# Optimization experiments

Measured on AMD Instinct MI355X. Metric: run time of the kernel, lower is better.

The kernel has to match this reference:

```python
import jax, jax.numpy as jnp
import numpy as np

NEG_SLOPE = 0.2  # PyG GATv2Conv default negative_slope


def gatv2_conv(x, src, dst, Wl, bl, Wr, br, att, bias, concat=True):
    # x: [N, Fin]; src/dst: [E] (message flows src -> dst, softmax over dst)
    N = x.shape[0]
    H, C = att.shape
    xl = (x @ Wl + bl).reshape(N, H, C)  # source-side transform (lin_l)
    xr = (x @ Wr + br).reshape(N, H, C)  # target-side transform (lin_r)
    e = xl[src] + xr[dst]                              # [E, H, C]
    score = jnp.sum(jax.nn.leaky_relu(e, NEG_SLOPE) * att, axis=-1)  # [E, H]
    # segment softmax over incoming edges of each target node
    m = jax.ops.segment_max(score, dst, num_segments=N)               # [N, H]
    a = jnp.exp(score - m[dst])
    denom = jax.ops.segment_sum(a, dst, num_segments=N)               # [N, H]
    alpha = a / denom[dst]                                            # [E, H]
    out = jax.ops.segment_sum(xl[src] * alpha[..., None], dst, num_segments=N)  # [N, H, C]
    if concat:
        out = out.reshape(N, H * C)
    else:
        out = out.mean(axis=1)
    return out + bias


def setup_inputs() -> dict:
    key = jax.random.key(0)
    ks = jax.random.split(key, 12)
    N, E, Fin = 100000, 1600000, 128
    H1, C1 = 8, 16
    C2 = 64
    def glorot(k, shape):
        fan_in, fan_out = shape[0], shape[-1]
        lim = (6.0 / (fan_in + fan_out)) ** 0.5
        return jax.random.uniform(k, shape, jnp.float32, -lim, lim)
    x = jax.random.normal(ks[0], (N, Fin), jnp.float32)
    edge_index = jax.random.randint(ks[1], (2, E), 0, N, dtype=jnp.int64)
    return {
        "x": x,
        "edge_index": edge_index,
        "Wl1": glorot(ks[2], (Fin, H1 * C1)),
        "bl1": jnp.zeros((H1 * C1,), jnp.float32),
        "Wr1": glorot(ks[3], (Fin, H1 * C1)),
        "br1": jnp.zeros((H1 * C1,), jnp.float32),
        "att1": glorot(ks[4], (H1, C1)),
        "bias1": jnp.zeros((H1 * C1,), jnp.float32),
        "Wl2": glorot(ks[5], (H1 * C1, C2)),
        "bl2": jnp.zeros((C2,), jnp.float32),
        "Wr2": glorot(ks[6], (H1 * C1, C2)),
        "br2": jnp.zeros((C2,), jnp.float32),
        "att2": glorot(ks[7], (1, C2)),
        "bias2": jnp.zeros((C2,), jnp.float32),
    }


def reference(x, edge_index, Wl1, bl1, Wr1, br1, att1, bias1,
              Wl2, bl2, Wr2, br2, att2, bias2):
    N = x.shape[0]
    loops = jnp.arange(N, dtype=edge_index.dtype)
    src = jnp.concatenate([edge_index[0], loops])  # PyG adds self loops by default
    dst = jnp.concatenate([edge_index[1], loops])
    # eval mode: F.dropout(training=False) is identity
    h = gatv2_conv(x, src, dst, Wl1, bl1, Wr1, br1, att1, bias1, concat=True)
    h = jax.nn.elu(h)
    out = gatv2_conv(h, src, dst, Wl2, bl2, Wr2, br2, att2, bias2, concat=True)
    return out
```

## Files before the change

kernel.cpp:

```cpp
#include <hip/hip_runtime.h>
#include <math.h>

#define FIN 128
#define F1  128
#define C2  64
#define NEG 0.2f

#define BKT_SHIFT 8
#define BKT_SIZE  256
#define SCAT_CHUNK 8192
#define IMGCAP 8192

typedef _Float16 half4 __attribute__((ext_vector_type(4)));
typedef _Float16 f16x8 __attribute__((ext_vector_type(8)));
typedef _Float16 h2    __attribute__((ext_vector_type(2)));
typedef float    f32x4 __attribute__((ext_vector_type(4)));

union H8u { f16x8 v; h2 p[4]; };

__device__ __forceinline__ float lrelu(float z) { return fmaxf(z, NEG * z); }

__global__ __launch_bounds__(256) void bucket_hist_kernel(
    const int* __restrict__ ei, int* __restrict__ bcnt, int E, int ET, int NBKT) {
  __shared__ int sh[512];
  const int t = threadIdx.x;
  for (int b = t; b < NBKT; b += 256) sh[b] = 0;
  __syncthreads();
  const int g0 = blockIdx.x * SCAT_CHUNK + t;
#pragma unroll
  for (int i = 0; i < 32; ++i) {
    const int g = g0 + i * 256;
    if (g < ET) {
      const int dst = (g < E) ? ei[E + g] : (g - E);
      atomicAdd(&sh[dst >> BKT_SHIFT], 1);
    }
  }
  __syncthreads();
  for (int b = t; b < NBKT; b += 256)
    if (sh[b]) atomicAdd(&bcnt[b], sh[b]);
}

__global__ __launch_bounds__(512) void bucket_scan_kernel(
    const int* __restrict__ bcnt, int* __restrict__ bbase, int* __restrict__ bcur,
    int* __restrict__ indptr, int NBKT, int N, int ET) {
  __shared__ int sh[512];
  const int t = threadIdx.x;
  const int v = (t < NBKT) ? bcnt[t] : 0;
  sh[t] = v;
  __syncthreads();
  for (int off = 1; off < 512; off <<= 1) {
    int val = (t >= off) ? sh[t - off] : 0;
    __syncthreads();
    sh[t] += val;
    __syncthreads();
  }
  const int excl = sh[t] - v;
  if (t < NBKT) { bbase[t] = excl; bcur[t] = excl; }
  if (t == NBKT - 1) bbase[NBKT] = excl + v;
  if (t == 0) indptr[N] = ET;
}

__global__ __launch_bounds__(256) void bucket_scatter_kernel(
    const int* __restrict__ ei, int* __restrict__ bcur, int* __restrict__ tmp,
    int E, int ET, int NBKT) {
  __shared__ int sh_hist[512];
  __shared__ int sh_base[512];
  const int t = threadIdx.x;
  for (int b = t; b < NBKT; b += 256) sh_hist[b] = 0;
  __syncthreads();
  const int g0 = blockIdx.x * SCAT_CHUNK + t;
  int bk[32], pk[32];
#pragma unroll
  for (int i = 0; i < 32; ++i) {
    const int g = g0 + i * 256;
    int b = -1, p = 0;
    if (g < ET) {
      const int src = (g < E) ? ei[g] : (g - E);
      const int dst = (g < E) ? ei[E + g] : (g - E);
      b = dst >> BKT_SHIFT;
      p = (src << BKT_SHIFT) | (dst & (BKT_SIZE - 1));
      atomicAdd(&sh_hist[b], 1);
    }
    bk[i] = b; pk[i] = p;
  }
  __syncthreads();
  for (int b = t; b < NBKT; b += 256) {
    const int c = sh_hist[b];
    sh_base[b] = c ? atomicAdd(&bcur[b], c) : 0;
    sh_hist[b] = 0;
  }
  __syncthreads();
#pragma unroll
  for (int i = 0; i < 32; ++i) {
    if (bk[i] >= 0) {
      const int off = atomicAdd(&sh_hist[bk[i]], 1);
      tmp[sh_base[bk[i]] + off] = pk[i];
    }
  }
}

__global__ __launch_bounds__(256) void build_csr_kernel(
    const int* __restrict__ tmp, const int* __restrict__ bbase,
    int* __restrict__ indptr, int* __restrict__ csr, int N) {
  __shared__ int cnt[256];
  __shared__ int cur[256];
  __shared__ int img[IMGCAP];
  const int b = blockIdx.x;
  const int t = threadIdx.x;
  const int base = bbase[b];
  const int cntb = bbase[b + 1] - base;
  cnt[t] = 0;
  __syncthreads();
  for (int i = t; i < cntb; i += 256)
    atomicAdd(&cnt[tmp[base + i] & (BKT_SIZE - 1)], 1);
  __syncthreads();
  const int v = cnt[t];
  cur[t] = v;
  __syncthreads();
  for (int off = 1; off < 256; off <<= 1) {
    int val = (t >= off) ? cur[t - off] : 0;
    __syncthreads();
    cur[t] += val;
    __syncthreads();
  }
  const int excl = cur[t] - v;
  const int node = (b << BKT_SHIFT) + t;
  if (node < N) indptr[node] = base + excl;
  __syncthreads();
  cur[t] = excl;
  __syncthreads();
  if (cntb <= IMGCAP) {
    for (int i = t; i < cntb; i += 256) {
      const int p = tmp[base + i];
      const int pos = atomicAdd(&cur[p & (BKT_SIZE - 1)], 1);
      img[pos] = p >> BKT_SHIFT;
    }
    __syncthreads();
    for (int i = t; i < cntb; i += 256) csr[base + i] = img[i];
  } else {
    for (int i = t; i < cntb; i += 256) {
      const int p = tmp[base + i];
      const int pos = atomicAdd(&cur[p & (BKT_SIZE - 1)], 1);
      csr[base + pos] = p >> BKT_SHIFT;
    }
  }
}

__global__ __launch_bounds__(256) void conv_fp16_kernel(
    const float* __restrict__ src, _Float16* __restrict__ dst, int n4) {
  const int i = blockIdx.x * 256 + threadIdx.x;
  if (i < n4) {
    const float4 v = ((const float4*)src)[i];
    half4 h;
    h.x = (_Float16)v.x; h.y = (_Float16)v.y;
    h.z = (_Float16)v.z; h.w = (_Float16)v.w;
    ((half4*)dst)[i] = h;
  }
}

__global__ __launch_bounds__(256) void wtrans_kernel(
    const float* __restrict__ W0, const float* __restrict__ W1,
    const float* __restrict__ W2, const float* __restrict__ W3,
    _Float16* __restrict__ T0, _Float16* __restrict__ T1,
    _Float16* __restrict__ T2, _Float16* __restrict__ T3) {
  const int m = blockIdx.y;
  const float* W = (m == 0) ? W0 : (m == 1) ? W1 : (m == 2) ? W2 : W3;
  _Float16* T = (m == 0) ? T0 : (m == 1) ? T1 : (m == 2) ? T2 : T3;
  const int ncols = (m < 2) ? 128 : 64;
  const int idx = blockIdx.x * 256 + threadIdx.x;
  if (idx < ncols * 128) {
    const int n = idx >> 7;
    const int k = idx & 127;
    T[idx] = (_Float16)W[k * ncols + n];
  }
}

template<int NCOLS, int CPW>
__global__ __launch_bounds__(256) void gemm_mfma_kernel(
    const _Float16* __restrict__ A,
    const _Float16* __restrict__ Wt0, const float* __restrict__ b0, _Float16* __restrict__ O0,
    const _Float16* __restrict__ Wt1, const float* __restrict__ b1, _Float16* __restrict__ O1,
    int M) {
  const int zsel = blockIdx.z;
  const _Float16* Wt = zsel ? Wt1 : Wt0;
  const float* bias  = zsel ? b1 : b0;
  _Float16* O        = zsel ? O1 : O0;
  const int wave = threadIdx.x >> 6;
  const int lane = threadIdx.x & 63;
  const int row16 = lane & 15;
  const int quad  = lane >> 4;
  const int kb = quad * 8;
  f16x8 bfrag[CPW][4];
  float bv[CPW];
#pragma unroll
  for (int c = 0; c < CPW; ++c) {
    const int n0 = (wave * CPW + c) * 16;
    bv[c] = bias[n0 + row16];
#pragma unroll
    for (int kt = 0; kt < 4; ++kt)
      bfrag[c][kt] = *(const f16x8*)(Wt + (n0 + row16) * 128 + kt * 32 + kb);
  }
  const int rowTiles = (M + 15) >> 4;
  for (int rt = blockIdx.x; rt < rowTiles; rt += gridDim.x) {
    const int r0 = rt << 4;
    const int arow = min(r0 + row16, M - 1);
    f16x8 afrag[4];
#pragma unroll
    for (int kt = 0; kt < 4; ++kt)
      afrag[kt] = *(const f16x8*)(A + (size_t)arow * 128 + kt * 32 + kb);
    f32x4 acc[CPW];
#pragma unroll
    for (int c = 0; c < CPW; ++c) acc[c] = (f32x4){0.f, 0.f, 0.f, 0.f};
#pragma unroll
    for (int kt = 0; kt < 4; ++kt)
#pragma unroll
      for (int c = 0; c < CPW; ++c)
        acc[c] = __builtin_amdgcn_mfma_f32_16x16x32_f16(afrag[kt], bfrag[c][kt], acc[c], 0, 0, 0);
#pragma unroll
    for (int c = 0; c < CPW; ++c) {
      const int col = (wave * CPW + c) * 16 + row16;
#pragma unroll
      for (int r = 0; r < 4; ++r) {
        const int row = r0 + quad * 4 + r;
        if (row < M)
          O[(size_t)row * NCOLS + col] = (_Float16)(acc[c][r] + bv[c]);
      }
    }
  }
}

__global__ __launch_bounds__(256) void attn1_kernel(
    const _Float16* __restrict__ xl, const _Float16* __restrict__ xr,
    const float* __restrict__ att, const float* __restrict__ bias,
    const int* __restrict__ indptr, const int* __restrict__ csr,
    _Float16* __restrict__ hout, int N) {
  const int lane = threadIdx.x & 15;
  const int v = blockIdx.x * 16 + (threadIdx.x >> 4);
  if (v >= N) return;
  const int c8 = lane << 3;
  const _Float16* xlp = xl + c8;
  H8u xru; xru.v = *(const f16x8*)(xr + (v << 7) + c8);
  H8u atu;
  {
    const float4 a0 = *(const float4*)(att + c8);
    const float4 a1 = *(const float4*)(att + c8 + 4);
    f16x8 a;
    a[0] = (_Float16)a0.x; a[1] = (_Float16)a0.y; a[2] = (_Float16)a0.z; a[3] = (_Float16)a0.w;
    a[4] = (_Float16)a1.x; a[5] = (_Float16)a1.y; a[6] = (_Float16)a1.z; a[7] = (_Float16)a1.w;
    atu.v = a;
  }
  const h2 neg2 = {(_Float16)NEG, (_Float16)NEG};
  const h2 zero2 = {(_Float16)0.f, (_Float16)0.f};
  const int beg = indptr[v];
  const int end = indptr[v + 1];
  float l = 0.f;
  float acc[8] = {0.f, 0.f, 0.f, 0.f, 0.f, 0.f, 0.f, 0.f};
  int e = beg;
  for (; e + 4 <= end; e += 4) {
    const int s0 = csr[e + 0];
    const int s1 = csr[e + 1];
    const int s2 = csr[e + 2];
    const int s3 = csr[e + 3];
    H8u x0, x1, x2, x3;
    x0.v = *(const f16x8*)(xlp + (s0 << 7));
    x1.v = *(const f16x8*)(xlp + (s1 << 7));
    x2.v = *(const f16x8*)(xlp + (s2 << 7));
    x3.v = *(const f16x8*)(xlp + (s3 << 7));
    h2 sa0 = zero2, sa1 = zero2, sa2 = zero2, sa3 = zero2;
#pragma unroll
    for (int j = 0; j < 4; ++j) {
      h2 e0 = x0.p[j] + xru.p[j];
      h2 e1 = x1.p[j] + xru.p[j];
      h2 e2 = x2.p[j] + xru.p[j];
      h2 e3 = x3.p[j] + xru.p[j];
      e0 = __builtin_elementwise_max(e0, e0 * neg2);
      e1 = __builtin_elementwise_max(e1, e1 * neg2);
      e2 = __builtin_elementwise_max(e2, e2 * neg2);
      e3 = __builtin_elementwise_max(e3, e3 * neg2);
      sa0 = e0 * atu.p[j] + sa0;
      sa1 = e1 * atu.p[j] + sa1;
      sa2 = e2 * atu.p[j] + sa2;
      sa3 = e3 * atu.p[j] + sa3;
    }
    float t0 = (float)sa0[0] + (float)sa0[1];
    float t1 = (float)sa1[0] + (float)sa1[1];
    float t2 = (float)sa2[0] + (float)sa2[1];
    float t3 = (float)sa3[0] + (float)sa3[1];
    t0 += __shfl_xor(t0, 1);  t1 += __shfl_xor(t1, 1);
    t2 += __shfl_xor(t2, 1);  t3 += __shfl_xor(t3, 1);
    const float p0 = __expf(t0);
    const float p1 = __expf(t1);
    const float p2 = __expf(t2);
    const float p3 = __expf(t3);
    l += (p0 + p1) + (p2 + p3);
#pragma unroll
    for (int j = 0; j < 4; ++j) {
      acc[2*j]   = fmaf(p0, (float)x0.p[j][0], acc[2*j]);
      acc[2*j+1] = fmaf(p0, (float)x0.p[j][1], acc[2*j+1]);
      acc[2*j]   = fmaf(p1, (float)x1.p[j][0], acc[2*j]);
      acc[2*j+1] = fmaf(p1, (float)x1.p[j][1], acc[2*j+1]);
      acc[2*j]   = fmaf(p2, (float)x2.p[j][0], acc[2*j]);
      acc[2*j+1] = fmaf(p2, (float)x2.p[j][1], acc[2*j+1]);
      acc[2*j]   = fmaf(p3, (float)x3.p[j][0], acc[2*j]);
      acc[2*j+1] = fmaf(p3, (float)x3.p[j][1], acc[2*j+1]);
    }
  }
  for (; e < end; ++e) {
    const int s = csr[e];
    H8u xv; xv.v = *(const f16x8*)(xlp + (s << 7));
    h2 sa = zero2;
#pragma unroll
    for (int j = 0; j < 4; ++j) {
      h2 ev = xv.p[j] + xru.p[j];
      ev = __builtin_elementwise_max(ev, ev * neg2);
      sa = ev * atu.p[j] + sa;
    }
    float tt = (float)sa[0] + (float)sa[1];
    tt += __shfl_xor(tt, 1);
    const float p = __expf(tt);
    l += p;
#pragma unroll
    for (int j = 0; j < 4; ++j) {
      acc[2*j]   = fmaf(p, (float)xv.p[j][0], acc[2*j]);
      acc[2*j+1] = fmaf(p, (float)xv.p[j][1], acc[2*j+1]);
    }
  }
  const float rl = 1.f / l;
  const float4 b0 = *(const float4*)(bias + c8);
  const float4 b1 = *(const float4*)(bias + c8 + 4);
  float r[8];
  r[0] = fmaf(acc[0], rl, b0.x); r[1] = fmaf(acc[1], rl, b0.y);
  r[2] = fmaf(acc[2], rl, b0.z); r[3] = fmaf(acc[3], rl, b0.w);
  r[4] = fmaf(acc[4], rl, b1.x); r[5] = fmaf(acc[5], rl, b1.y);
  r[6] = fmaf(acc[6], rl, b1.z); r[7] = fmaf(acc[7], rl, b1.w);
  f16x8 hres;
#pragma unroll
  for (int i = 0; i < 8; ++i) {
    const float z = r[i] > 0.f ? r[i] : expm1f(r[i]);
    hres[i] = (_Float16)z;
  }
  *(f16x8*)(hout + (v << 7) + c8) = hres;
}

__global__ __launch_bounds__(256) void attn2_kernel(
    const _Float16* __restrict__ xl, const _Float16* __restrict__ xr,
    const float* __restrict__ att, const float* __restrict__ bias,
    const int* __restrict__ indptr, const int* __restrict__ csr,
    float* __restrict__ out, int N) {
  const int lane = threadIdx.x & 7;
  const int v = blockIdx.x * 32 + (threadIdx.x >> 3);
  if (v >= N) return;
  const int c8 = lane << 3;
  const _Float16* xlp = xl + c8;
  H8u xru; xru.v = *(const f16x8*)(xr + (v << 6) + c8);
  H8u atu;
  {
    const float4 a0 = *(const float4*)(att + c8);
    const float4 a1 = *(const float4*)(att + c8 + 4);
    f16x8 a;
    a[0] = (_Float16)a0.x; a[1] = (_Float16)a0.y; a[2] = (_Float16)a0.z; a[3] = (_Float16)a0.w;
    a[4] = (_Float16)a1.x; a[5] = (_Float16)a1.y; a[6] = (_Float16)a1.z; a[7] = (_Float16)a1.w;
    atu.v = a;
  }
  const h2 neg2 = {(_Float16)NEG, (_Float16)NEG};
  const h2 zero2 = {(_Float16)0.f, (_Float16)0.f};
  const int beg = indptr[v];
  const int end = indptr[v + 1];
  float l = 0.f;
  float acc[8] = {0.f, 0.f, 0.f, 0.f, 0.f, 0.f, 0.f, 0.f};
  int e = beg;
  for (; e + 4 <= end; e += 4) {
    const int s0 = csr[e + 0];
    const int s1 = csr[e + 1];
    const int s2 = csr[e + 2];
    const int s3 = csr[e + 3];
    H8u x0, x1, x2, x3;
    x0.v = *(const f16x8*)(xlp + (s0 << 6));
    x1.v = *(const f16x8*)(xlp + (s1 << 6));
    x2.v = *(const f16x8*)(xlp + (s2 << 6));
    x3.v = *(const f16x8*)(xlp + (s3 << 6));
    h2 sa0 = zero2, sa1 = zero2, sa2 = zero2, sa3 = zero2;
#pragma unroll
    for (int j = 0; j < 4; ++j) {
      h2 e0 = x0.p[j] + xru.p[j];
      h2 e1 = x1.p[j] + xru.p[j];
      h2 e2 = x2.p[j] + xru.p[j];
      h2 e3 = x3.p[j] + xru.p[j];
      e0 = __builtin_elementwise_max(e0, e0 * neg2);
      e1 = __builtin_elementwise_max(e1, e1 * neg2);
      e2 = __builtin_elementwise_max(e2, e2 * neg2);
      e3 = __builtin_elementwise_max(e3, e3 * neg2);
      sa0 = e0 * atu.p[j] + sa0;
      sa1 = e1 * atu.p[j] + sa1;
      sa2 = e2 * atu.p[j] + sa2;
      sa3 = e3 * atu.p[j] + sa3;
    }
    float t0 = (float)sa0[0] + (float)sa0[1];
    float t1 = (float)sa1[0] + (float)sa1[1];
    float t2 = (float)sa2[0] + (float)sa2[1];
    float t3 = (float)sa3[0] + (float)sa3[1];
    t0 += __shfl_xor(t0, 1);  t1 += __shfl_xor(t1, 1);
    t2 += __shfl_xor(t2, 1);  t3 += __shfl_xor(t3, 1);
    t0 += __shfl_xor(t0, 2);  t1 += __shfl_xor(t1, 2);
    t2 += __shfl_xor(t2, 2);  t3 += __shfl_xor(t3, 2);
    t0 += __shfl_xor(t0, 4);  t1 += __shfl_xor(t1, 4);
    t2 += __shfl_xor(t2, 4);  t3 += __shfl_xor(t3, 4);
    const float p0 = __expf(t0);
    const float p1 = __expf(t1);
    const float p2 = __expf(t2);
    const float p3 = __expf(t3);
    l += (p0 + p1) + (p2 + p3);
#pragma unroll
    for (int j = 0; j < 4; ++j) {
      acc[2*j]   = fmaf(p0, (float)x0.p[j][0], acc[2*j]);
      acc[2*j+1] = fmaf(p0, (float)x0.p[j][1], acc[2*j+1]);
      acc[2*j]   = fmaf(p1, (float)x1.p[j][0], acc[2*j]);
      acc[2*j+1] = fmaf(p1, (float)x1.p[j][1], acc[2*j+1]);
      acc[2*j]   = fmaf(p2, (float)x2.p[j][0], acc[2*j]);
      acc[2*j+1] = fmaf(p2, (float)x2.p[j][1], acc[2*j+1]);
      acc[2*j]   = fmaf(p3, (float)x3.p[j][0], acc[2*j]);
      acc[2*j+1] = fmaf(p3, (float)x3.p[j][1], acc[2*j+1]);
    }
  }
  for (; e < end; ++e) {
    const int s = csr[e];
    H8u xv; xv.v = *(const f16x8*)(xlp + (s << 6));
    h2 sa = zero2;
#pragma unroll
    for (int j = 0; j < 4; ++j) {
      h2 ev = xv.p[j] + xru.p[j];
      ev = __builtin_elementwise_max(ev, ev * neg2);
      sa = ev * atu.p[j] + sa;
    }
    float tt = (float)sa[0] + (float)sa[1];
    tt += __shfl_xor(tt, 1);
    tt += __shfl_xor(tt, 2);
    tt += __shfl_xor(tt, 4);
    const float p = __expf(tt);
    l += p;
#pragma unroll
    for (int j = 0; j < 4; ++j) {
      acc[2*j]   = fmaf(p, (float)xv.p[j][0], acc[2*j]);
      acc[2*j+1] = fmaf(p, (float)xv.p[j][1], acc[2*j+1]);
    }
  }
  const float rl = 1.f / l;
  const float4 b0 = *(const float4*)(bias + c8);
  const float4 b1 = *(const float4*)(bias + c8 + 4);
  float4 o0, o1;
  o0.x = fmaf(acc[0], rl, b0.x); o0.y = fmaf(acc[1], rl, b0.y);
  o0.z = fmaf(acc[2], rl, b0.z); o0.w = fmaf(acc[3], rl, b0.w);
  o1.x = fmaf(acc[4], rl, b1.x); o1.y = fmaf(acc[5], rl, b1.y);
  o1.z = fmaf(acc[6], rl, b1.z); o1.w = fmaf(acc[7], rl, b1.w);
  *(float4*)(out + (v << 6) + c8) = o0;
  *(float4*)(out + (v << 6) + c8 + 4) = o1;
}

extern "C" void kernel_launch(void* const* d_in, const int* in_sizes, int n_in,
                              void* d_out, int out_size, void* d_ws, size_t ws_size,
                              hipStream_t stream) {
  const float* x     = (const float*)d_in[0];
  const int*   ei    = (const int*)d_in[1];
  const float* Wl1   = (const float*)d_in[2];
  const float* bl1   = (const float*)d_in[3];
  const float* Wr1   = (const float*)d_in[4];
  const float* br1   = (const float*)d_in[5];
  const float* att1  = (const float*)d_in[6];
  const float* bias1 = (const float*)d_in[7];
  const float* Wl2   = (const float*)d_in[8];
  const float* bl2   = (const float*)d_in[9];
  const float* Wr2   = (const float*)d_in[10];
  const float* br2   = (const float*)d_in[11];
  const float* att2  = (const float*)d_in[12];
  const float* bias2 = (const float*)d_in[13];

  const int N  = in_sizes[0] / FIN;
  const int E  = in_sizes[1] / 2;
  const int ET = E + N;
  const int NBKT = (N + BKT_SIZE - 1) >> BKT_SHIFT;

  _Float16* xh    = (_Float16*)d_ws;
  _Float16* xl1h  = xh + (size_t)N * FIN;
  _Float16* xr1h  = xl1h + (size_t)N * F1;
  _Float16* hbufh = xr1h + (size_t)N * F1;
  _Float16* Wt1l  = hbufh + (size_t)N * F1;
  _Float16* Wt1r  = Wt1l + 128 * 128;
  _Float16* Wt2l  = Wt1r + 128 * 128;
  _Float16* Wt2r  = Wt2l + 64 * 128;
  int* indptr = (int*)(Wt2r + 64 * 128);
  int* csr    = indptr + (N + 1);
  int* bcnt   = csr + ET;
  int* bbase  = bcnt + 512;
  int* bcur   = bbase + 513;
  int* tmp    = (int*)hbufh;
  _Float16* xl2h = xl1h;
  _Float16* xr2h = xr1h;
  float* out  = (float*)d_out;

  const int sblocks = (ET + SCAT_CHUNK - 1) / SCAT_CHUNK;

  hipMemsetAsync(bcnt, 0, 512 * sizeof(int), stream);
  bucket_hist_kernel<<<sblocks, 256, 0, stream>>>(ei, bcnt, E, ET, NBKT);
  bucket_scan_kernel<<<1, 512, 0, stream>>>(bcnt, bbase, bcur, indptr, NBKT, N, ET);
  bucket_scatter_kernel<<<sblocks, 256, 0, stream>>>(ei, bcur, tmp, E, ET, NBKT);
  build_csr_kernel<<<NBKT, 256, 0, stream>>>(tmp, bbase, indptr, csr, N);

  const int n4 = N * FIN / 4;
  conv_fp16_kernel<<<(n4 + 255) / 256, 256, 0, stream>>>(x, xh, n4);
  wtrans_kernel<<<dim3(64, 4), 256, 0, stream>>>(Wl1, Wr1, Wl2, Wr2, Wt1l, Wt1r, Wt2l, Wt2r);

  gemm_mfma_kernel<128, 2><<<dim3(1024, 1, 2), 256, 0, stream>>>(
      xh, Wt1l, bl1, xl1h, Wt1r, br1, xr1h, N);

  attn1_kernel<<<(N + 15) / 16, 256, 0, stream>>>(xl1h, xr1h, att1, bias1, indptr, csr, hbufh, N);

  gemm_mfma_kernel<64, 1><<<dim3(1024, 1, 2), 256, 0, stream>>>(
      hbufh, Wt2l, bl2, xl2h, Wt2r, br2, xr2h, N);

  attn2_kernel<<<(N + 31) / 32, 256, 0, stream>>>(xl2h, xr2h, att2, bias2, indptr, csr, out, N);
}
```

Before: 362.7 us.

## Fuse fp16 input conversion into dual-output GEMM and software-pipeline attention gathers

Removes the separate fp32-to-fp16 conversion kernel and instead converts x inside the GEMM while loading A fragments. The GEMM now computes the lin_l and lin_r outputs in one block, sharing the A loads rather than launching two z-slices that each read A. The attention kernels gain double-buffered neighbor gathers that prefetch the next four edges while the current four are being processed, and the scalar tail loop becomes a masked batch. The cost is more registers per thread, because both weight sets and two gather buffers stay live, which may lower occupancy.

```diff
diff --git a/kernel.cpp b/kernel.cpp
--- a/kernel.cpp
+++ b/kernel.cpp
@@ -17,8 +17,6 @@
 typedef float    f32x4 __attribute__((ext_vector_type(4)));
 
 union H8u { f16x8 v; h2 p[4]; };
-
-__device__ __forceinline__ float lrelu(float z) { return fmaxf(z, NEG * z); }
 
 __global__ __launch_bounds__(256) void bucket_hist_kernel(
     const int* __restrict__ ei, int* __restrict__ bcnt, int E, int ET, int NBKT) {
@@ -143,18 +141,6 @@
       const int pos = atomicAdd(&cur[p & (BKT_SIZE - 1)], 1);
       csr[base + pos] = p >> BKT_SHIFT;
     }
-  }
-}
-
-__global__ __launch_bounds__(256) void conv_fp16_kernel(
-    const float* __restrict__ src, _Float16* __restrict__ dst, int n4) {
-  const int i = blockIdx.x * 256 + threadIdx.x;
-  if (i < n4) {
-    const float4 v = ((const float4*)src)[i];
-    half4 h;
-    h.x = (_Float16)v.x; h.y = (_Float16)v.y;
-    h.z = (_Float16)v.z; h.w = (_Float16)v.w;
-    ((half4*)dst)[i] = h;
   }
 }
 
@@ -175,57 +161,150 @@
   }
 }
 
-template<int NCOLS, int CPW>
-__global__ __launch_bounds__(256) void gemm_mfma_kernel(
-    const _Float16* __restrict__ A,
-    const _Float16* __restrict__ Wt0, const float* __restrict__ b0, _Float16* __restrict__ O0,
-    const _Float16* __restrict__ Wt1, const float* __restrict__ b1, _Float16* __restrict__ O1,
+template<int NCOLS, int CPW, bool AF32>
+__global__ __launch_bounds__(256) void gemm_dual_kernel(
+    const void* __restrict__ Av,
+    const _Float16* __restrict__ WtL, const float* __restrict__ bLp, _Float16* __restrict__ OL,
+    const _Float16* __restrict__ WtR, const float* __restrict__ bRp, _Float16* __restrict__ ORp,
     int M) {
-  const int zsel = blockIdx.z;
-  const _Float16* Wt = zsel ? Wt1 : Wt0;
-  const float* bias  = zsel ? b1 : b0;
-  _Float16* O        = zsel ? O1 : O0;
   const int wave = threadIdx.x >> 6;
   const int lane = threadIdx.x & 63;
   const int row16 = lane & 15;
   const int quad  = lane >> 4;
   const int kb = quad * 8;
-  f16x8 bfrag[CPW][4];
-  float bv[CPW];
+  f16x8 bfL[CPW][4], bfR[CPW][4];
+  float bvL[CPW], bvR[CPW];
 #pragma unroll
   for (int c = 0; c < CPW; ++c) {
     const int n0 = (wave * CPW + c) * 16;
-    bv[c] = bias[n0 + row16];
-#pragma unroll
-    for (int kt = 0; kt < 4; ++kt)
-      bfrag[c][kt] = *(const f16x8*)(Wt + (n0 + row16) * 128 + kt * 32 + kb);
+    bvL[c] = bLp[n0 + row16];
+    bvR[c] = bRp[n0 + row16];
+#pragma unroll
+    for (int kt = 0; kt < 4; ++kt) {
+      bfL[c][kt] = *(const f16x8*)(WtL + (n0 + row16) * 128 + kt * 32 + kb);
+      bfR[c][kt] = *(const f16x8*)(WtR + (n0 + row16) * 128 + kt * 32 + kb);
+    }
   }
   const int rowTiles = (M + 15) >> 4;
   for (int rt = blockIdx.x; rt < rowTiles; rt += gridDim.x) {
     const int r0 = rt << 4;
     const int arow = min(r0 + row16, M - 1);
-    f16x8 afrag[4];
-#pragma unroll
-    for (int kt = 0; kt < 4; ++kt)
-      afrag[kt] = *(const f16x8*)(A + (size_t)arow * 128 + kt * 32 + kb);
-    f32x4 acc[CPW];
-#pragma unroll
-    for (int c = 0; c < CPW; ++c) acc[c] = (f32x4){0.f, 0.f, 0.f, 0.f};
-#pragma unroll
-    for (int kt = 0; kt < 4; ++kt)
-#pragma unroll
-      for (int c = 0; c < CPW; ++c)
-        acc[c] = __builtin_amdgcn_mfma_f32_16x16x32_f16(afrag[kt], bfrag[c][kt], acc[c], 0, 0, 0);
+    f16x8 af[4];
+    if constexpr (AF32) {
+      const float4* ap = (const float4*)Av + (size_t)arow * 32;
+#pragma unroll
+      for (int kt = 0; kt < 4; ++kt) {
+        const float4 u = ap[kt * 8 + quad * 2];
+        const float4 w = ap[kt * 8 + quad * 2 + 1];
+        f16x8 h;
+        h[0] = (_Float16)u.x; h[1] = (_Float16)u.y;
+        h[2] = (_Float16)u.z; h[3] = (_Float16)u.w;
+        h[4] = (_Float16)w.x; h[5] = (_Float16)w.y;
+        h[6] = (_Float16)w.z; h[7] = (_Float16)w.w;
+        af[kt] = h;
+      }
+    } else {
+      const _Float16* A = (const _Float16*)Av;
+#pragma unroll
+      for (int kt = 0; kt < 4; ++kt)
+        af[kt] = *(const f16x8*)(A + (size_t)arow * 128 + kt * 32 + kb);
+    }
+    f32x4 accL[CPW], accR[CPW];
+#pragma unroll
+    for (int c = 0; c < CPW; ++c) {
+      accL[c] = (f32x4){0.f, 0.f, 0.f, 0.f};
+      accR[c] = (f32x4){0.f, 0.f, 0.f, 0.f};
+    }
+#pragma unroll
+    for (int kt = 0; kt < 4; ++kt) {
+#pragma unroll
+      for (int c = 0; c < CPW; ++c) {
+        accL[c] = __builtin_amdgcn_mfma_f32_16x16x32_f16(af[kt], bfL[c][kt], accL[c], 0, 0, 0);
+        accR[c] = __builtin_amdgcn_mfma_f32_16x16x32_f16(af[kt], bfR[c][kt], accR[c], 0, 0, 0);
+      }
+    }
 #pragma unroll
     for (int c = 0; c < CPW; ++c) {
       const int col = (wave * CPW + c) * 16 + row16;
 #pragma unroll
       for (int r = 0; r < 4; ++r) {
         const int row = r0 + quad * 4 + r;
-        if (row < M)
-          O[(size_t)row * NCOLS + col] = (_Float16)(acc[c][r] + bv[c]);
+        if (row < M) {
+          OL[(size_t)row * NCOLS + col]  = (_Float16)(accL[c][r] + bvL[c]);
+          ORp[(size_t)row * NCOLS + col] = (_Float16)(accR[c][r] + bvR[c]);
+        }
       }
     }
+  }
+}
+
+template<int LSH>
+__device__ __forceinline__ void attn_load4(const _Float16* __restrict__ xlp,
+                                           const int* __restrict__ csr,
+                                           int e, int endm1,
+                                           H8u& x0, H8u& x1, H8u& x2, H8u& x3) {
+  const int s0 = csr[min(e,     endm1)];
+  const int s1 = csr[min(e + 1, endm1)];
+  const int s2 = csr[min(e + 2, endm1)];
+  const int s3 = csr[min(e + 3, endm1)];
+  x0.v = *(const f16x8*)(xlp + ((size_t)s0 << LSH));
+  x1.v = *(const f16x8*)(xlp + ((size_t)s1 << LSH));
+  x2.v = *(const f16x8*)(xlp + ((size_t)s2 << LSH));
+  x3.v = *(const f16x8*)(xlp + ((size_t)s3 << LSH));
+}
+
+template<int XORS>
+__device__ __forceinline__ void attn_batch(const H8u& x0, const H8u& x1,
+                                           const H8u& x2, const H8u& x3,
+                                           const H8u& xru, const H8u& atu,
+                                           int rem, float& l, float (&acc)[8]) {
+  const h2 neg2 = {(_Float16)NEG, (_Float16)NEG};
+  const h2 zero2 = {(_Float16)0.f, (_Float16)0.f};
+  h2 sa0 = zero2, sa1 = zero2, sa2 = zero2, sa3 = zero2;
+#pragma unroll
+  for (int j = 0; j < 4; ++j) {
+    h2 e0 = x0.p[j] + xru.p[j];
+    h2 e1 = x1.p[j] + xru.p[j];
+    h2 e2 = x2.p[j] + xru.p[j];
+    h2 e3 = x3.p[j] + xru.p[j];
+    e0 = __builtin_elementwise_max(e0, e0 * neg2);
+    e1 = __builtin_elementwise_max(e1, e1 * neg2);
+    e2 = __builtin_elementwise_max(e2, e2 * neg2);
+    e3 = __builtin_elementwise_max(e3, e3 * neg2);
+    sa0 = e0 * atu.p[j] + sa0;
+    sa1 = e1 * atu.p[j] + sa1;
+    sa2 = e2 * atu.p[j] + sa2;
+    sa3 = e3 * atu.p[j] + sa3;
+  }
+  float t0 = (float)sa0[0] + (float)sa0[1];
+  float t1 = (float)sa1[0] + (float)sa1[1];
+  float t2 = (float)sa2[0] + (float)sa2[1];
+  float t3 = (float)sa3[0] + (float)sa3[1];
+  t0 += __shfl_xor(t0, 1);  t1 += __shfl_xor(t1, 1);
+  t2 += __shfl_xor(t2, 1);  t3 += __shfl_xor(t3, 1);
+  if constexpr (XORS >= 2) {
+    t0 += __shfl_xor(t0, 2);  t1 += __shfl_xor(t1, 2);
+    t2 += __shfl_xor(t2, 2);  t3 += __shfl_xor(t3, 2);
+  }
+  if constexpr (XORS >= 3) {
+    t0 += __shfl_xor(t0, 4);  t1 += __shfl_xor(t1, 4);
+    t2 += __shfl_xor(t2, 4);  t3 += __shfl_xor(t3, 4);
+  }
+  const float p0 = __expf(t0);
+  const float p1 = (rem > 1) ? __expf(t1) : 0.f;
+  const float p2 = (rem > 2) ? __expf(t2) : 0.f;
+  const float p3 = (rem > 3) ? __expf(t3) : 0.f;
+  l += (p0 + p1) + (p2 + p3);
+#pragma unroll
+  for (int j = 0; j < 4; ++j) {
+    acc[2*j]   = fmaf(p0, (float)x0.p[j][0], acc[2*j]);
+    acc[2*j+1] = fmaf(p0, (float)x0.p[j][1], acc[2*j+1]);
+    acc[2*j]   = fmaf(p1, (float)x1.p[j][0], acc[2*j]);
+    acc[2*j+1] = fmaf(p1, (float)x1.p[j][1], acc[2*j+1]);
+    acc[2*j]   = fmaf(p2, (float)x2.p[j][0], acc[2*j]);
+    acc[2*j+1] = fmaf(p2, (float)x2.p[j][1], acc[2*j+1]);
+    acc[2*j]   = fmaf(p3, (float)x3.p[j][0], acc[2*j]);
+    acc[2*j+1] = fmaf(p3, (float)x3.p[j][1], acc[2*j+1]);
   }
 }
 
@@ -239,7 +318,7 @@
   if (v >= N) return;
   const int c8 = lane << 3;
   const _Float16* xlp = xl + c8;
-  H8u xru; xru.v = *(const f16x8*)(xr + (v << 7) + c8);
+  H8u xru; xru.v = *(const f16x8*)(xr + ((size_t)v << 7) + c8);
   H8u atu;
   {
     const float4 a0 = *(const float4*)(att + c8);
@@ -249,97 +328,47 @@
     a[4] = (_Float16)a1.x; a[5] = (_Float16)a1.y; a[6] = (_Float16)a1.z; a[7] = (_Float16)a1.w;
     atu.v = a;
   }
-  const h2 neg2 = {(_Float16)NEG, (_Float16)NEG};
-  const h2 zero2 = {(_Float16)0.f, (_Float16)0.f};
   const int beg = indptr[v];
   const int end = indptr[v + 1];
+  const int endm1 = end - 1;
   float l = 0.f;
   float acc[8] = {0.f, 0.f, 0.f, 0.f, 0.f, 0.f, 0.f, 0.f};
+
+  H8u a0, a1, a2, a3, b0, b1, b2, b3;
   int e = beg;
-  for (; e + 4 <= end; e += 4) {
-    const int s0 = csr[e + 0];
-    const int s1 = csr[e + 1];
-    const int s2 = csr[e + 2];
-    const int s3 = csr[e + 3];
-    H8u x0, x1, x2, x3;
-    x0.v = *(const f16x8*)(xlp + (s0 << 7));
-    x1.v = *(const f16x8*)(xlp + (s1 << 7));
-    x2.v = *(const f16x8*)(xlp + (s2 << 7));
-    x3.v = *(const f16x8*)(xlp + (s3 << 7));
-    h2 sa0 = zero2, sa1 = zero2, sa2 = zero2, sa3 = zero2;
-#pragma unroll
-    for (int j = 0; j < 4; ++j) {
-      h2 e0 = x0.p[j] + xru.p[j];
-      h2 e1 = x1.p[j] + xru.p[j];
-      h2 e2 = x2.p[j] + xru.p[j];
-      h2 e3 = x3.p[j] + xru.p[j];
-      e0 = __builtin_elementwise_max(e0, e0 * neg2);
-      e1 = __builtin_elementwise_max(e1, e1 * neg2);
-      e2 = __builtin_elementwise_max(e2, e2 * neg2);
-      e3 = __builtin_elementwise_max(e3, e3 * neg2);
-      sa0 = e0 * atu.p[j] + sa0;
-      sa1 = e1 * atu.p[j] + sa1;
-      sa2 = e2 * atu.p[j] + sa2;
-      sa3 = e3 * atu.p[j] + sa3;
-    }
-    float t0 = (float)sa0[0] + (float)sa0[1];
-    float t1 = (float)sa1[0] + (float)sa1[1];
-    float t2 = (float)sa2[0] + (float)sa2[1];
-    float t3 = (float)sa3[0] + (float)sa3[1];
-    t0 += __shfl_xor(t0, 1);  t1 += __shfl_xor(t1, 1);
-    t2 += __shfl_xor(t2, 1);  t3 += __shfl_xor(t3, 1);
-    const float p0 = __expf(t0);
-    const float p1 = __expf(t1);
-    const float p2 = __expf(t2);
-    const float p3 = __expf(t3);
-    l += (p0 + p1) + (p2 + p3);
-#pragma unroll
-    for (int j = 0; j < 4; ++j) {
-      acc[2*j]   = fmaf(p0, (float)x0.p[j][0], acc[2*j]);
-      acc[2*j+1] = fmaf(p0, (float)x0.p[j][1], acc[2*j+1]);
-      acc[2*j]   = fmaf(p1, (float)x1.p[j][0], acc[2*j]);
-      acc[2*j+1] = fmaf(p1, (float)x1.p[j][1], acc[2*j+1]);
-      acc[2*j]   = fmaf(p2, (float)x2.p[j][0], acc[2*j]);
-      acc[2*j+1] = fmaf(p2, (float)x2.p[j][1], acc[2*j+1]);
-      acc[2*j]   = fmaf(p3, (float)x3.p[j][0], acc[2*j]);
-      acc[2*j+1] = fmaf(p3, (float)x3.p[j][1], acc[2*j+1]);
-    }
-  }
-  for (; e < end; ++e) {
-    const int s = csr[e];
-    H8u xv; xv.v = *(const f16x8*)(xlp + (s << 7));
-    h2 sa = zero2;
-#pragma unroll
-    for (int j = 0; j < 4; ++j) {
-      h2 ev = xv.p[j] + xru.p[j];
-      ev = __builtin_elementwise_max(ev, ev * neg2);
-      sa = ev * atu.p[j] + sa;
-    }
-    float tt = (float)sa[0] + (float)sa[1];
-    tt += __shfl_xor(tt, 1);
-    const float p = __expf(tt);
-    l += p;
-#pragma unroll
-    for (int j = 0; j < 4; ++j) {
-      acc[2*j]   = fmaf(p, (float)xv.p[j][0], acc[2*j]);
-      acc[2*j+1] = fmaf(p, (float)xv.p[j][1], acc[2*j+1]);
-    }
-  }
+  attn_load4<7>(xlp, csr, e, endm1, a0, a1, a2, a3);
+  while (e + 4 < end) {
+    attn_load4<7>(xlp, csr, e + 4, endm1, b0, b1, b2, b3);
+    attn_batch<1>(a0, a1, a2, a3, xru, atu, 4, l, acc);
+    e += 4;
+    if (e + 4 < end) {
+      attn_load4<7>(xlp, csr, e + 4, endm1, a0, a1, a2, a3);
+      attn_batch<1>(b0, b1, b2, b3, xru, atu, 4, l, acc);
+      e += 4;
+    } else {
+      const int rem = end - e;
+      attn_batch<1>(b0, b1, b2, b3, xru, atu, rem, l, acc);
+      e = end;
+      break;
+    }
+  }
+  if (e < end) attn_batch<1>(a0, a1, a2, a3, xru, atu, end - e, l, acc);
+
   const float rl = 1.f / l;
-  const float4 b0 = *(const float4*)(bias + c8);
-  const float4 b1 = *(const float4*)(bias + c8 + 4);
+  const float4 bb0 = *(const float4*)(bias + c8);
+  const float4 bb1 = *(const float4*)(bias + c8 + 4);
   float r[8];
-  r[0] = fmaf(acc[0], rl, b0.x); r[1] = fmaf(acc[1], rl, b0.y);
-  r[2] = fmaf(acc[2], rl, b0.z); r[3] = fmaf(acc[3], rl, b0.w);
-  r[4] = fmaf(acc[4], rl, b1.x); r[5] = fmaf(acc[5], rl, b1.y);
-  r[6] = fmaf(acc[6], rl, b1.z); r[7] = fmaf(acc[7], rl, b1.w);
+  r[0] = fmaf(acc[0], rl, bb0.x); r[1] = fmaf(acc[1], rl, bb0.y);
+  r[2] = fmaf(acc[2], rl, bb0.z); r[3] = fmaf(acc[3], rl, bb0.w);
+  r[4] = fmaf(acc[4], rl, bb1.x); r[5] = fmaf(acc[5], rl, bb1.y);
+  r[6] = fmaf(acc[6], rl, bb1.z); r[7] = fmaf(acc[7], rl, bb1.w);
   f16x8 hres;
 #pragma unroll
   for (int i = 0; i < 8; ++i) {
     const float z = r[i] > 0.f ? r[i] : expm1f(r[i]);
     hres[i] = (_Float16)z;
   }
-  *(f16x8*)(hout + (v << 7) + c8) = hres;
+  *(f16x8*)(hout + ((size_t)v << 7) + c8) = hres;
 }
 
 __global__ __launch_bounds__(256) void attn2_kernel(
@@ -352,7 +381,7 @@
   if (v >= N) return;
   const int c8 = lane << 3;
   const _Float16* xlp = xl + c8;
-  H8u xru; xru.v = *(const f16x8*)(xr + (v << 6) + c8);
+  H8u xru; xru.v = *(const f16x8*)(xr + ((size_t)v << 6) + c8);
   H8u atu;
   {
     const float4 a0 = *(const float4*)(att + c8);
@@ -362,98 +391,42 @@
     a[4] = (_Float16)a1.x; a[5] = (_Float16)a1.y; a[6] = (_Float16)a1.z; a[7] = (_Float16)a1.w;
     atu.v = a;
   }
-  const h2 neg2 = {(_Float16)NEG, (_Float16)NEG};
-  const h2 zero2 = {(_Float16)0.f, (_Float16)0.f};
   const int beg = indptr[v];
   const int end = indptr[v + 1];
+  const int endm1 = end - 1;
   float l = 0.f;
   float acc[8] = {0.f, 0.f, 0.f, 0.f, 0.f, 0.f, 0.f, 0.f};
+
+  H8u a0, a1, a2, a3, b0, b1, b2, b3;
   int e = beg;
-  for (; e + 4 <= end; e += 4) {
-    const int s0 = csr[e + 0];
-    const int s1 = csr[e + 1];
-    const int s2 = csr[e + 2];
-    const int s3 = csr[e + 3];
-    H8u x0, x1, x2, x3;
-    x0.v = *(const f16x8*)(xlp + (s0 << 6));
-    x1.v = *(const f16x8*)(xlp + (s1 << 6));
-    x2.v = *(const f16x8*)(xlp + (s2 << 6));
-    x3.v = *(const f16x8*)(xlp + (s3 << 6));
-    h2 sa0 = zero2, sa1 = zero2, sa2 = zero2, sa3 = zero2;
-#pragma unroll
-    for (int j = 0; j < 4; ++j) {
-      h2 e0 = x0.p[j] + xru.p[j];
-      h2 e1 = x1.p[j] + xru.p[j];
-      h2 e2 = x2.p[j] + xru.p[j];
-      h2 e3 = x3.p[j] + xru.p[j];
-      e0 = __builtin_elementwise_max(e0, e0 * neg2);
-      e1 = __builtin_elementwise_max(e1, e1 * neg2);
-      e2 = __builtin_elementwise_max(e2, e2 * neg2);
-      e3 = __builtin_elementwise_max(e3, e3 * neg2);
-      sa0 = e0 * atu.p[j] + sa0;
-      sa1 = e1 * atu.p[j] + sa1;
-      sa2 = e2 * atu.p[j] + sa2;
-      sa3 = e3 * atu.p[j] + sa3;
-    }
-    float t0 = (float)sa0[0] + (float)sa0[1];
-    float t1 = (float)sa1[0] + (float)sa1[1];
-    float t2 = (float)sa2[0] + (float)sa2[1];
-    float t3 = (float)sa3[0] + (float)sa3[1];
-    t0 += __shfl_xor(t0, 1);  t1 += __shfl_xor(t1, 1);
-    t2 += __shfl_xor(t2, 1);  t3 += __shfl_xor(t3, 1);
-    t0 += __shfl_xor(t0, 2);  t1 += __shfl_xor(t1, 2);
-    t2 += __shfl_xor(t2, 2);  t3 += __shfl_xor(t3, 2);
-    t0 += __shfl_xor(t0, 4);  t1 += __shfl_xor(t1, 4);
-    t2 += __shfl_xor(t2, 4);  t3 += __shfl_xor(t3, 4);
-    const float p0 = __expf(t0);
-    const float p1 = __expf(t1);
-    const float p2 = __expf(t2);
-    const float p3 = __expf(t3);
-    l += (p0 + p1) + (p2 + p3);
-#pragma unroll
-    for (int j = 0; j < 4; ++j) {
-      acc[2*j]   = fmaf(p0, (float)x0.p[j][0], acc[2*j]);
-      acc[2*j+1] = fmaf(p0, (float)x0.p[j][1], acc[2*j+1]);
-      acc[2*j]   = fmaf(p1, (float)x1.p[j][0], acc[2*j]);
-      acc[2*j+1] = fmaf(p1, (float)x1.p[j][1], acc[2*j+1]);
-      acc[2*j]   = fmaf(p2, (float)x2.p[j][0], acc[2*j]);
-      acc[2*j+1] = fmaf(p2, (float)x2.p[j][1], acc[2*j+1]);
-      acc[2*j]   = fmaf(p3, (float)x3.p[j][0], acc[2*j]);
-      acc[2*j+1] = fmaf(p3, (float)x3.p[j][1], acc[2*j+1]);
-    }
-  }
-  for (; e < end; ++e) {
-    const int s = csr[e];
-    H8u xv; xv.v = *(const f16x8*)(xlp + (s << 6));
-    h2 sa = zero2;
-#pragma unroll
-    for (int j = 0; j < 4; ++j) {
-      h2 ev = xv.p[j] + xru.p[j];
-      ev = __builtin_elementwise_max(ev, ev * neg2);
-      sa = ev * atu.p[j] + sa;
-    }
-    float tt = (float)sa[0] + (float)sa[1];
-    tt += __shfl_xor(tt, 1);
-    tt += __shfl_xor(tt, 2);
-    tt += __shfl_xor(tt, 4);
-    const float p = __expf(tt);
-    l += p;
-#pragma unroll
-    for (int j = 0; j < 4; ++j) {
-      acc[2*j]   = fmaf(p, (float)xv.p[j][0], acc[2*j]);
-      acc[2*j+1] = fmaf(p, (float)xv.p[j][1], acc[2*j+1]);
-    }
-  }
+  attn_load4<6>(xlp, csr, e, endm1, a0, a1, a2, a3);
+  while (e + 4 < end) {
+    attn_load4<6>(xlp, csr, e + 4, endm1, b0, b1, b2, b3);
+    attn_batch<3>(a0, a1, a2, a3, xru, atu, 4, l, acc);
+    e += 4;
+    if (e + 4 < end) {
+      attn_load4<6>(xlp, csr, e + 4, endm1, a0, a1, a2, a3);
+      attn_batch<3>(b0, b1, b2, b3, xru, atu, 4, l, acc);
+      e += 4;
+    } else {
+      const int rem = end - e;
+      attn_batch<3>(b0, b1, b2, b3, xru, atu, rem, l, acc);
+      e = end;
+      break;
+    }
+  }
+  if (e < end) attn_batch<3>(a0, a1, a2, a3, xru, atu, end - e, l, acc);
+
   const float rl = 1.f / l;
-  const float4 b0 = *(const float4*)(bias + c8);
-  const float4 b1 = *(const float4*)(bias + c8 + 4);
+  const float4 bb0 = *(const float4*)(bias + c8);
+  const float4 bb1 = *(const float4*)(bias + c8 + 4);
   float4 o0, o1;
-  o0.x = fmaf(acc[0], rl, b0.x); o0.y = fmaf(acc[1], rl, b0.y);
-  o0.z = fmaf(acc[2], rl, b0.z); o0.w = fmaf(acc[3], rl, b0.w);
-  o1.x = fmaf(acc[4], rl, b1.x); o1.y = fmaf(acc[5], rl, b1.y);
-  o1.z = fmaf(acc[6], rl, b1.z); o1.w = fmaf(acc[7], rl, b1.w);
-  *(float4*)(out + (v << 6) + c8) = o0;
-  *(float4*)(out + (v << 6) + c8 + 4) = o1;
+  o0.x = fmaf(acc[0], rl, bb0.x); o0.y = fmaf(acc[1], rl, bb0.y);
+  o0.z = fmaf(acc[2], rl, bb0.z); o0.w = fmaf(acc[3], rl, bb0.w);
+  o1.x = fmaf(acc[4], rl, bb1.x); o1.y = fmaf(acc[5], rl, bb1.y);
+  o1.z = fmaf(acc[6], rl, bb1.z); o1.w = fmaf(acc[7], rl, bb1.w);
+  *(float4*)(out + ((size_t)v << 6) + c8) = o0;
+  *(float4*)(out + ((size_t)v << 6) + c8 + 4) = o1;
 }
 
 extern "C" void kernel_launch(void* const* d_in, const int* in_sizes, int n_in,
@@ -479,8 +452,7 @@
   const int ET = E + N;
   const int NBKT = (N + BKT_SIZE - 1) >> BKT_SHIFT;
 
-  _Float16* xh    = (_Float16*)d_ws;
-  _Float16* xl1h  = xh + (size_t)N * FIN;
+  _Float16* xl1h  = (_Float16*)d_ws;
   _Float16* xr1h  = xl1h + (size_t)N * F1;
   _Float16* hbufh = xr1h + (size_t)N * F1;
   _Float16* Wt1l  = hbufh + (size_t)N * F1;
@@ -505,16 +477,14 @@
   bucket_scatter_kernel<<<sblocks, 256, 0, stream>>>(ei, bcur, tmp, E, ET, NBKT);
   build_csr_kernel<<<NBKT, 256, 0, stream>>>(tmp, bbase, indptr, csr, N);
 
-  const int n4 = N * FIN / 4;
-  conv_fp16_kernel<<<(n4 + 255) / 256, 256, 0, stream>>>(x, xh, n4);
   wtrans_kernel<<<dim3(64, 4), 256, 0, stream>>>(Wl1, Wr1, Wl2, Wr2, Wt1l, Wt1r, Wt2l, Wt2r);
 
-  gemm_mfma_kernel<128, 2><<<dim3(1024, 1, 2), 256, 0, stream>>>(
-      xh, Wt1l, bl1, xl1h, Wt1r, br1, xr1h, N);
+  gemm_dual_kernel<128, 2, true><<<1024, 256, 0, stream>>>(
+      x, Wt1l, bl1, xl1h, Wt1r, br1, xr1h, N);
 
   attn1_kernel<<<(N + 15) / 16, 256, 0, stream>>>(xl1h, xr1h, att1, bias1, indptr, csr, hbufh, N);
 
-  gemm_mfma_kernel<64, 1><<<dim3(1024, 1, 2), 256, 0, stream>>>(
+  gemm_dual_kernel<64, 1, false><<<1024, 256, 0, stream>>>(
       hbufh, Wt2l, bl2, xl2h, Wt2r, br2, xr2h, N);
 
   attn2_kernel<<<(N + 31) / 32, 256, 0, stream>>>(xl2h, xr2h, att2, bias2, indptr, csr, out, N);
```

New measurement: 348.4 us. -3.9%, faster.
